# Optimization experiments

Hardware: AMD Instinct MI355X
Metric: run time of the kernel (lower is better)

## Reference

```python
import jax, jax.numpy as jnp
import numpy as np

B, NF, N, D, S, H = 16, 16, 1024, 128, 8, 128
EPS = 1e-8
SCALE = D ** -0.5


def _ln(x, g, b):
    m = x.mean(-1, keepdims=True)
    v = ((x - m) ** 2).mean(-1, keepdims=True)
    return (x - m) / jnp.sqrt(v + 1e-5) * g + b


def setup_inputs() -> dict:
    key = jax.random.key(0)
    ks = jax.random.split(key, 16)
    w = lambda k, *s: jax.random.normal(k, s, jnp.float32) * 0.02
    return {
        'inputs': jax.random.normal(ks[0], (B, NF, N, D), jnp.float32),
        'slots_init': jax.random.normal(ks[1], (1, S, D), jnp.float32),
        'Wq': w(ks[2], D, D), 'bq': jnp.zeros((D,), jnp.float32),
        'Wk': w(ks[3], D, D), 'bk': jnp.zeros((D,), jnp.float32),
        'Wv': w(ks[4], D, D), 'bv': jnp.zeros((D,), jnp.float32),
        'W1': w(ks[5], H, D), 'b1': jnp.zeros((H,), jnp.float32),
        'W2': w(ks[6], D, H), 'b2': jnp.zeros((D,), jnp.float32),
        'Wih': w(ks[7], 3 * D, D), 'Whh': w(ks[8], 3 * D, D),
        'bih': jnp.zeros((3 * D,), jnp.float32), 'bhh': jnp.zeros((3 * D,), jnp.float32),
        'g_in': jnp.ones((D,), jnp.float32), 'be_in': jnp.zeros((D,), jnp.float32),
        'g_sl': jnp.ones((D,), jnp.float32), 'be_sl': jnp.zeros((D,), jnp.float32),
        'g_ff': jnp.ones((D,), jnp.float32), 'be_ff': jnp.zeros((D,), jnp.float32),
    }


def reference(inputs, slots_init, Wq, bq, Wk, bk, Wv, bv, W1, b1, W2, b2,
              Wih, Whh, bih, bhh, g_in, be_in, g_sl, be_sl, g_ff, be_ff):
    def gru(x, h):  # PyTorch GRUCell, x/h: [BS, D]
        gi = x @ Wih.T + bih
        gh = h @ Whh.T + bhh
        r = jax.nn.sigmoid(gi[:, :D] + gh[:, :D])
        z = jax.nn.sigmoid(gi[:, D:2 * D] + gh[:, D:2 * D])
        n = jnp.tanh(gi[:, 2 * D:] + r * gh[:, 2 * D:])
        return (1.0 - z) * n + z * h

    def get_attention(slots, x):  # slots [B,S,D], x [B,N,D]
        slots_prev = slots
        xn = _ln(x, g_in, be_in)
        k = xn @ Wk.T + bk
        v = xn @ Wv.T + bv
        q = _ln(slots, g_sl, be_sl) @ Wq.T + bq
        dots = jnp.einsum('bid,bjd->bij', q, k) * SCALE  # [B,S,N]
        attn_ori = jax.nn.softmax(dots, axis=1) + EPS    # softmax over slots
        attn = attn_ori / attn_ori.sum(axis=-1, keepdims=True)
        updates = jnp.einsum('bjd,bij->bid', v, attn)    # [B,S,D]
        slots = gru(updates.reshape(-1, D), slots_prev.reshape(-1, D)).reshape(slots.shape[0], -1, D)
        ff = jax.nn.relu(_ln(slots, g_ff, be_ff) @ W1.T + b1) @ W2.T + b2
        return slots + ff, attn_ori

    slots = jnp.broadcast_to(slots_init, (inputs.shape[0], S, D))
    slots, _ = get_attention(slots, inputs[:, 0])  # warm-up on frame 0

    def body(carry, x_f):
        s, a = get_attention(carry, x_f)
        return s, (s, a)

    _, (slots_seq, attn_seq) = jax.lax.scan(body, slots, jnp.moveaxis(inputs, 1, 0))
    slots_out = jnp.moveaxis(slots_seq, 0, 1)  # [B,NF,S,D]
    attns = jnp.moveaxis(attn_seq, 0, 1)       # [B,NF,S,N]
    return slots_out, attns
```

## Files before the change

kernel.cpp:

```cpp
#include <hip/hip_runtime.h>

#define B_ 16
#define NF_ 16
#define N_ 1024
#define D_ 128
#define S_ 8
#define SCALE_ 0.08838834764831845f
#define NB 256
#define NT 512

struct SmemA {
  float Xt[64 * 132];
  float qWs[1024];
  float at[512];
  float rowsum[64], rowsum2[64];
  float qbs[8];
};
struct SmemB {
  float Pk[128];
  float gh[384];
  float gi[384];
  float hn[128], buf[128], hid[128], nrm[128];
  float red[8];
  float ssm;
};
union Smem { SmemA a; SmemB b; };

__device__ __forceinline__ float gload(const float* p) {
  return __hip_atomic_load(p, __ATOMIC_RELAXED, __HIP_MEMORY_SCOPE_AGENT);
}
__device__ __forceinline__ void gstore(float* p, float v) {
  __hip_atomic_store(p, v, __ATOMIC_RELAXED, __HIP_MEMORY_SCOPE_AGENT);
}

__device__ __forceinline__ void arrive(unsigned* c) {
  __syncthreads();
  if (threadIdx.x == 0) {
    __builtin_amdgcn_s_waitcnt(0);
    __hip_atomic_fetch_add(c, 1u, __ATOMIC_RELAXED, __HIP_MEMORY_SCOPE_AGENT);
  }
}
__device__ __forceinline__ void wait_for(unsigned* c, unsigned target) {
  if (threadIdx.x == 0) {
    while (__hip_atomic_load(c, __ATOMIC_RELAXED, __HIP_MEMORY_SCOPE_AGENT) < target)
      __builtin_amdgcn_s_sleep(1);
  }
  __syncthreads();
}

__device__ __forceinline__ float dot128f(const float* __restrict__ wrow, const float* x, float acc) {
  const float4* w = (const float4*)wrow;
#pragma unroll
  for (int i = 0; i < 32; ++i) {
    float4 v = w[i];
    const float4 xv = *(const float4*)(x + i * 4);
    acc += v.x * xv.x + v.y * xv.y + v.z * xv.z + v.w * xv.w;
  }
  return acc;
}

__device__ __forceinline__ void stats128(float v, int t, float* red, float& m, float& inv, float eps) {
  __syncthreads();
  float s = (t < 128) ? v : 0.f;
  float s2 = (t < 128) ? v * v : 0.f;
#pragma unroll
  for (int off = 32; off; off >>= 1) { s += __shfl_down(s, off); s2 += __shfl_down(s2, off); }
  if (t == 0)  { red[0] = s; red[2] = s2; }
  if (t == 64) { red[1] = s; red[3] = s2; }
  __syncthreads();
  m = (red[0] + red[1]) * (1.f / 128.f);
  float var = (red[2] + red[3]) * (1.f / 128.f) - m * m;
  inv = rsqrtf(var + 1e-5f);
}

__device__ __forceinline__ float sigm(float x) { return 1.f / (1.f + __expf(-x)); }
__device__ __forceinline__ float tanh_f(float x) { return 1.f - 2.f / (1.f + __expf(2.f * x)); }

__device__ void q_project(SmemB& Bm, const float* slot,
    const float* __restrict__ g_sl, const float* __restrict__ be_sl,
    const float* __restrict__ Wqk, const float* __restrict__ bqk,
    const float* __restrict__ wqbk, const float* __restrict__ bqbk,
    float* qW_g, float* qb_g, int bs) {
  int t = threadIdx.x;
  float m, inv;
  float sv = (t < 128) ? slot[t] : 0.f;
  stats128(sv, t, Bm.red, m, inv, 1e-5f);
  if (t < 128) Bm.nrm[t] = (sv - m) * inv * g_sl[t] + be_sl[t];
  __syncthreads();
  if (t < 128) {
    float a = dot128f(Wqk + t * 128, Bm.nrm, bqk[t]);
    gstore(&qW_g[bs * 128 + t], a);
    float p = wqbk[t] * Bm.nrm[t];
#pragma unroll
    for (int off = 32; off; off >>= 1) p += __shfl_down(p, off);
    if (t == 0)  Bm.red[4] = p;
    if (t == 64) Bm.red[5] = p;
  }
  __syncthreads();
  if (t == 0) gstore(&qb_g[bs], Bm.red[4] + Bm.red[5] + bqbk[0]);
}

__global__ __launch_bounds__(128) void precomp(
    const float* __restrict__ Wih, const float* __restrict__ bih,
    const float* __restrict__ Wv, const float* __restrict__ bv,
    const float* __restrict__ Wq, const float* __restrict__ bq,
    const float* __restrict__ Wk, const float* __restrict__ bk,
    float* Wiv, float* bihv, float* Wqk, float* bqk, float* wqbk, float* bqbk) {
  __shared__ float r2[2];
  int r = blockIdx.x, t = threadIdx.x;
  if (r < 384) {
    float acc = 0.f;
#pragma unroll 8
    for (int k = 0; k < 128; ++k) acc += Wih[r * 128 + k] * Wv[k * 128 + t];
    Wiv[r * 128 + t] = acc;
    float p = Wih[r * 128 + t] * bv[t];
#pragma unroll
    for (int off = 32; off; off >>= 1) p += __shfl_down(p, off);
    if ((t & 63) == 0) r2[t >> 6] = p;
    __syncthreads();
    if (t == 0) bihv[r] = r2[0] + r2[1] + bih[r];
  } else {
    int c = r - 384;
    float acc = 0.f;
#pragma unroll 8
    for (int dd = 0; dd < 128; ++dd) acc += Wk[dd * 128 + c] * Wq[dd * 128 + t];
    Wqk[c * 128 + t] = acc;
    float p = Wk[t * 128 + c] * bq[t];
#pragma unroll
    for (int off = 32; off; off >>= 1) p += __shfl_down(p, off);
    if ((t & 63) == 0) r2[t >> 6] = p;
    __syncthreads();
    if (t == 0) bqk[c] = r2[0] + r2[1];
    if (c == 0) {
      float a2 = 0.f;
#pragma unroll 8
      for (int dd = 0; dd < 128; ++dd) a2 += Wq[dd * 128 + t] * bk[dd];
      wqbk[t] = a2;
      float p2 = bq[t] * bk[t];
#pragma unroll
      for (int off = 32; off; off >>= 1) p2 += __shfl_down(p2, off);
      __syncthreads();
      if ((t & 63) == 0) r2[t >> 6] = p2;
      __syncthreads();
      if (t == 0) bqbk[0] = r2[0] + r2[1];
    }
  }
}

__global__ __launch_bounds__(NT) void slot_persist(
    const float* __restrict__ x, const float* __restrict__ slots_init,
    const float* __restrict__ Whh, const float* __restrict__ bhh,
    const float* __restrict__ W1, const float* __restrict__ b1,
    const float* __restrict__ W2, const float* __restrict__ b2,
    const float* __restrict__ g_in, const float* __restrict__ be_in,
    const float* __restrict__ g_sl, const float* __restrict__ be_sl,
    const float* __restrict__ g_ff, const float* __restrict__ be_ff,
    const float* __restrict__ Wiv, const float* __restrict__ bihv,
    const float* __restrict__ Wqk, const float* __restrict__ bqk,
    const float* __restrict__ wqbk, const float* __restrict__ bqbk,
    float* out_slots, float* out_attn,
    unsigned* cntA, unsigned* cntB,
    float* qW_g, float* qb_g, float* P_part, float* S_part) {
  __shared__ __align__(16) Smem sm;
  __shared__ __align__(16) float slot_sh[128];
  __shared__ __align__(16) float gs[128], bs_[128];
  int t = threadIdx.x, bid = blockIdx.x;
  int b = bid >> 4, jt = bid & 15;
  bool isB = (jt < 8);
  unsigned* cA = cntA + (b << 6);
  unsigned* cB = cntB + (b << 6);

  if (t < 128) { gs[t] = g_in[t]; bs_[t] = be_in[t]; }
  if (isB) {
    if (t < 128) slot_sh[t] = slots_init[jt * 128 + t];
    q_project(sm.b, slot_sh, g_sl, be_sl, Wqk, bqk, wqbk, bqbk, qW_g, qb_g, b * 8 + jt);
    arrive(cB);
  }
  float4 pf[4];
  {
    const float* xsrc = x + (((long)b * NF_ + 0) * N_ + jt * 64) * D_;
#pragma unroll
    for (int i = 0; i < 4; ++i) {
      int ch = t + i * 512;
      pf[i] = *(const float4*)(xsrc + (ch >> 5) * 128 + (ch & 31) * 4);
    }
  }
  wait_for(cB, 8u);

  for (int it = 0; it < 17; ++it) {
    int f = (it == 0) ? 0 : it - 1;
    int wo = it > 0;
#pragma unroll
    for (int i = 0; i < 4; ++i) {
      int ch = t + i * 512;
      *(float4*)&sm.a.Xt[(ch >> 5) * 132 + (ch & 31) * 4] = pf[i];
    }
    sm.a.qWs[t] = gload(&qW_g[b * 1024 + t]);
    sm.a.qWs[512 + t] = gload(&qW_g[b * 1024 + 512 + t]);
    if (t < 8) sm.a.qbs[t] = gload(&qb_g[b * 8 + t]);
    __syncthreads();
    int r8 = t >> 3, p8 = t & 7;
    {
      const float4* row4 = (const float4*)(sm.a.Xt + r8 * 132 + p8 * 16);
      float s1 = 0.f, s2 = 0.f;
#pragma unroll
      for (int i = 0; i < 4; ++i) {
        float4 v = row4[i];
        s1 += v.x + v.y + v.z + v.w;
        s2 += v.x * v.x + v.y * v.y + v.z * v.z + v.w * v.w;
      }
      s1 += __shfl_down(s1, 1); s2 += __shfl_down(s2, 1);
      s1 += __shfl_down(s1, 2); s2 += __shfl_down(s2, 2);
      s1 += __shfl_down(s1, 4); s2 += __shfl_down(s2, 4);
      if (p8 == 0) { sm.a.rowsum[r8] = s1; sm.a.rowsum2[r8] = s2; }
    }
    __syncthreads();
    {
      float m = sm.a.rowsum[r8] * (1.f / 128.f);
      float var = sm.a.rowsum2[r8] * (1.f / 128.f) - m * m;
      float inv = rsqrtf(var + 1e-5f);
      float4* row4 = (float4*)(sm.a.Xt + r8 * 132 + p8 * 16);
      const float4* gg4 = (const float4*)(gs + p8 * 16);
      const float4* bb4 = (const float4*)(bs_ + p8 * 16);
#pragma unroll
      for (int i = 0; i < 4; ++i) {
        float4 v = row4[i], g4 = gg4[i], b4 = bb4[i];
        v.x = (v.x - m) * inv * g4.x + b4.x;
        v.y = (v.y - m) * inv * g4.y + b4.y;
        v.z = (v.z - m) * inv * g4.z + b4.z;
        v.w = (v.w - m) * inv * g4.w + b4.w;
        row4[i] = v;
      }
    }
    __syncthreads();
    {
      int s = t >> 6, j = t & 63;
      const float4* qq4 = (const float4*)(sm.a.qWs + s * 128);
      const float4* xr4 = (const float4*)(sm.a.Xt + j * 132);
      float d = 0.f;
#pragma unroll
      for (int k = 0; k < 32; ++k) {
        float4 xv = xr4[k], qv = qq4[k];
        d += xv.x * qv.x + xv.y * qv.y + xv.z * qv.z + xv.w * qv.w;
      }
      sm.a.at[s * 64 + j] = (d + sm.a.qbs[s]) * SCALE_;
    }
    __syncthreads();
    if (t < 64) {
      float vals[8], mx = -1e30f;
#pragma unroll
      for (int s = 0; s < 8; ++s) { vals[s] = sm.a.at[s * 64 + t]; mx = fmaxf(mx, vals[s]); }
      float sum = 0.f;
#pragma unroll
      for (int s = 0; s < 8; ++s) { vals[s] = __expf(vals[s] - mx); sum += vals[s]; }
      float rr = 1.f / sum;
#pragma unroll
      for (int s = 0; s < 8; ++s) { vals[s] = vals[s] * rr + 1e-8f; sm.a.at[s * 64 + t] = vals[s]; }
      if (wo) {
#pragma unroll
        for (int s = 0; s < 8; ++s)
          out_attn[(((long)b * NF_ + f) * S_ + s) * N_ + jt * 64 + t] = vals[s];
      }
    }
    __syncthreads();
    {
      int w = t >> 6, lane = t & 63;
      float v = sm.a.at[w * 64 + lane];
#pragma unroll
      for (int off = 32; off; off >>= 1) v += __shfl_down(v, off);
      if (lane == 0) gstore(&S_part[(b * 16 + jt) * 8 + w], v);
    }
    {
      int k2 = t & 127, h = t >> 7;
      float u0 = 0.f, u1 = 0.f;
      const float* a0 = sm.a.at + h * 64;
      const float* a1 = sm.a.at + (h + 4) * 64;
#pragma unroll
      for (int j0 = 0; j0 < 64; j0 += 4) {
        float4 av0 = *(const float4*)(a0 + j0);
        float4 av1 = *(const float4*)(a1 + j0);
        float x0 = sm.a.Xt[(j0 + 0) * 132 + k2];
        float x1 = sm.a.Xt[(j0 + 1) * 132 + k2];
        float x2 = sm.a.Xt[(j0 + 2) * 132 + k2];
        float x3 = sm.a.Xt[(j0 + 3) * 132 + k2];
        u0 += av0.x * x0 + av0.y * x1 + av0.z * x2 + av0.w * x3;
        u1 += av1.x * x0 + av1.y * x1 + av1.z * x2 + av1.w * x3;
      }
      float* pp = P_part + (long)(b * 16 + jt) * 8 * 128;
      gstore(&pp[h * 128 + k2], u0);
      gstore(&pp[(h + 4) * 128 + k2], u1);
    }
    arrive(cA);
    if (it < 16) {
      const float* xsrc = x + (((long)b * NF_ + it) * N_ + jt * 64) * D_;
#pragma unroll
      for (int i = 0; i < 4; ++i) {
        int ch = t + i * 512;
        pf[i] = *(const float4*)(xsrc + (ch >> 5) * 128 + (ch & 31) * 4);
      }
    }
    if (isB) {
      wait_for(cA, 16u * (it + 1));
      SmemB& Bm = sm.b;
      int s = jt;
      if (t < 128) {
        float pa = 0.f;
#pragma unroll
        for (int j = 0; j < 16; ++j)
          pa += gload(&P_part[(long)((b * 16 + j) * 8 + s) * 128 + t]);
        Bm.Pk[t] = pa;
      } else {
        int r = t - 128;
        Bm.gh[r] = dot128f(Whh + r * 128, slot_sh, bhh[r]);
      }
      __syncthreads();
      if (t < 384) {
        Bm.gi[t] = dot128f(Wiv + (long)t * 128, Bm.Pk, 0.f);
      } else if (t >= 448 && t < 464) {
        int tl = t - 448;
        float sv = gload(&S_part[(b * 16 + tl) * 8 + s]);
        sv += __shfl_down(sv, 8); sv += __shfl_down(sv, 4);
        sv += __shfl_down(sv, 2); sv += __shfl_down(sv, 1);
        if (tl == 0) Bm.ssm = sv;
      }
      __syncthreads();
      if (t < 128) {
        float invss = 1.f / Bm.ssm;
        float gr = sigm(Bm.gi[t] * invss + bihv[t] + Bm.gh[t]);
        float gz = sigm(Bm.gi[128 + t] * invss + bihv[128 + t] + Bm.gh[128 + t]);
        float gn = tanh_f(Bm.gi[256 + t] * invss + bihv[256 + t] + gr * Bm.gh[256 + t]);
        Bm.hn[t] = (1.f - gz) * gn + gz * slot_sh[t];
      }
      float m, inv;
      float hv = (t < 128) ? Bm.hn[t] : 0.f;
      stats128(hv, t, Bm.red, m, inv, 1e-5f);
      if (t < 128) Bm.buf[t] = (hv - m) * inv * g_ff[t] + be_ff[t];
      __syncthreads();
      if (t < 128) Bm.hid[t] = fmaxf(dot128f(W1 + t * 128, Bm.buf, b1[t]), 0.f);
      __syncthreads();
      if (t < 128) {
        float ffv = dot128f(W2 + t * 128, Bm.hid, b2[t]);
        float sn = Bm.hn[t] + ffv;
        slot_sh[t] = sn;
        if (wo) out_slots[(((long)b * NF_ + f) * S_ + s) * D_ + t] = sn;
      }
      __syncthreads();
      if (it < 16) {
        q_project(Bm, slot_sh, g_sl, be_sl, Wqk, bqk, wqbk, bqbk, qW_g, qb_g, b * 8 + s);
        arrive(cB);
        wait_for(cB, 8u * (it + 2));
      }
    } else {
      if (it < 16) wait_for(cB, 8u * (it + 2));
    }
  }
}

extern "C" void kernel_launch(void* const* d_in, const int* in_sizes, int n_in,
                              void* d_out, int out_size, void* d_ws, size_t ws_size,
                              hipStream_t stream) {
  const float* inputs     = (const float*)d_in[0];
  const float* slots_init = (const float*)d_in[1];
  const float* Wq  = (const float*)d_in[2];
  const float* bq  = (const float*)d_in[3];
  const float* Wk  = (const float*)d_in[4];
  const float* bk  = (const float*)d_in[5];
  const float* Wv  = (const float*)d_in[6];
  const float* bv  = (const float*)d_in[7];
  const float* W1  = (const float*)d_in[8];
  const float* b1  = (const float*)d_in[9];
  const float* W2  = (const float*)d_in[10];
  const float* b2  = (const float*)d_in[11];
  const float* Wih = (const float*)d_in[12];
  const float* Whh = (const float*)d_in[13];
  const float* bih = (const float*)d_in[14];
  const float* bhh = (const float*)d_in[15];
  const float* g_in  = (const float*)d_in[16];
  const float* be_in = (const float*)d_in[17];
  const float* g_sl  = (const float*)d_in[18];
  const float* be_sl = (const float*)d_in[19];
  const float* g_ff  = (const float*)d_in[20];
  const float* be_ff = (const float*)d_in[21];

  float* out_slots = (float*)d_out;
  float* out_attn  = out_slots + (size_t)B_ * NF_ * S_ * D_;

  char* ws = (char*)d_ws;
  unsigned* cntA = (unsigned*)ws;
  unsigned* cntB = (unsigned*)(ws + 4096);
  float* Wiv   = (float*)(ws + 16384);
  float* bihv  = (float*)(ws + 212992);
  float* WqkW  = (float*)(ws + 214528);
  float* bqk   = (float*)(ws + 280064);
  float* wqbk  = (float*)(ws + 280576);
  float* bqbk  = (float*)(ws + 281088);
  float* qW_g  = (float*)(ws + 281344);
  float* qb_g  = (float*)(ws + 346880);
  float* P_part = (float*)(ws + 347392);
  float* S_part = (float*)(ws + 1395968);

  hipMemsetAsync(d_ws, 0, 16384, stream);

  precomp<<<512, 128, 0, stream>>>(Wih, bih, Wv, bv, Wq, bq, Wk, bk,
                                   Wiv, bihv, WqkW, bqk, wqbk, bqbk);
  slot_persist<<<NB, NT, 0, stream>>>(inputs, slots_init, Whh, bhh,
      W1, b1, W2, b2, g_in, be_in, g_sl, be_sl, g_ff, be_ff,
      Wiv, bihv, WqkW, bqk, wqbk, bqbk,
      out_slots, out_attn, cntA, cntB, qW_g, qb_g, P_part, S_part);
}
```

Before: 716.9 us.

## Fold input LayerNorm into query and update reductions, use atomic accumulation

Instead of normalizing each 64x128 input tile in shared memory, the kernel folds the LayerNorm gain into the published query vector. It applies per-row mean and rstd algebraically in the dot product and in the weighted update sum. Row statistics are computed straight from the prefetched registers, and the tile is stored with an XOR swizzle instead of padding. Per-block partial updates are accumulated with atomics into double-buffered global arrays, so the slot blocks no longer sum 16 partials. The wait for new queries moves to the top of the next iteration so the next frame's prefetch overlaps the GRU/MLP phase. The trade-off is more atomic traffic and a larger workspace memset.

```diff
diff --git a/kernel.cpp b/kernel.cpp
--- a/kernel.cpp
+++ b/kernel.cpp
@@ -10,21 +10,19 @@
 #define NT 512
 
 struct SmemA {
-  float Xt[64 * 132];
-  float qWs[1024];
-  float at[512];
-  float rowsum[64], rowsum2[64];
-  float qbs[8];
+  float Xt[64 * 128];
+  float at[8 * 64];
+  float gqWs[1024];
+  float mean[64], rinv[64];
+  float c1s[8], c0s[8];
 };
 struct SmemB {
   float Pk[128];
   float gh[384];
   float gi[384];
   float hn[128], buf[128], hid[128], nrm[128];
-  float red[8];
-  float ssm;
+  float red[16];
 };
-union Smem { SmemA a; SmemB b; };
 
 __device__ __forceinline__ float gload(const float* p) {
   return __hip_atomic_load(p, __ATOMIC_RELAXED, __HIP_MEMORY_SCOPE_AGENT);
@@ -32,7 +30,6 @@
 __device__ __forceinline__ void gstore(float* p, float v) {
   __hip_atomic_store(p, v, __ATOMIC_RELAXED, __HIP_MEMORY_SCOPE_AGENT);
 }
-
 __device__ __forceinline__ void arrive(unsigned* c) {
   __syncthreads();
   if (threadIdx.x == 0) {
@@ -76,28 +73,64 @@
 __device__ __forceinline__ float sigm(float x) { return 1.f / (1.f + __expf(-x)); }
 __device__ __forceinline__ float tanh_f(float x) { return 1.f - 2.f / (1.f + __expf(2.f * x)); }
 
-__device__ void q_project(SmemB& Bm, const float* slot,
+__device__ __forceinline__ void stage_stats(const float4* pf, float* Xt, float* mean, float* rinv, int t) {
+  float s1[4], s2[4];
+#pragma unroll
+  for (int i = 0; i < 4; ++i) {
+    int r = (t >> 5) + i * 16, kg = t & 31;
+    *(float4*)&Xt[r * 128 + ((kg ^ (r & 7)) << 2)] = pf[i];
+    s1[i] = pf[i].x + pf[i].y + pf[i].z + pf[i].w;
+    s2[i] = pf[i].x * pf[i].x + pf[i].y * pf[i].y + pf[i].z * pf[i].z + pf[i].w * pf[i].w;
+  }
+#pragma unroll
+  for (int mk = 16; mk; mk >>= 1) {
+#pragma unroll
+    for (int i = 0; i < 4; ++i) { s1[i] += __shfl_xor(s1[i], mk); s2[i] += __shfl_xor(s2[i], mk); }
+  }
+  if ((t & 31) == 0) {
+#pragma unroll
+    for (int i = 0; i < 4; ++i) {
+      int r = (t >> 5) + i * 16;
+      float mm = s1[i] * (1.f / 128.f);
+      mean[r] = mm;
+      rinv[r] = rsqrtf(s2[i] * (1.f / 128.f) - mm * mm + 1e-5f);
+    }
+  }
+}
+
+__device__ void q_project_pub(SmemB& Bm, const float* slot,
     const float* __restrict__ g_sl, const float* __restrict__ be_sl,
     const float* __restrict__ Wqk, const float* __restrict__ bqk,
     const float* __restrict__ wqbk, const float* __restrict__ bqbk,
-    float* qW_g, float* qb_g, int bs) {
-  int t = threadIdx.x;
+    const float* gI, const float* bI,
+    float* gqW_g, float* cc_g, int b, int s, int t) {
   float m, inv;
   float sv = (t < 128) ? slot[t] : 0.f;
   stats128(sv, t, Bm.red, m, inv, 1e-5f);
   if (t < 128) Bm.nrm[t] = (sv - m) * inv * g_sl[t] + be_sl[t];
   __syncthreads();
   if (t < 128) {
-    float a = dot128f(Wqk + t * 128, Bm.nrm, bqk[t]);
-    gstore(&qW_g[bs * 128 + t], a);
-    float p = wqbk[t] * Bm.nrm[t];
-#pragma unroll
-    for (int off = 32; off; off >>= 1) p += __shfl_down(p, off);
-    if (t == 0)  Bm.red[4] = p;
-    if (t == 64) Bm.red[5] = p;
-  }
-  __syncthreads();
-  if (t == 0) gstore(&qb_g[bs], Bm.red[4] + Bm.red[5] + bqbk[0]);
+    float qv = dot128f(Wqk + t * 128, Bm.nrm, bqk[t]);
+    float gq = gI[t] * qv;
+    gstore(&gqW_g[b * 1024 + s * 128 + t], gq);
+    float r0 = gq, r1 = bI[t] * qv, r2 = wqbk[t] * Bm.nrm[t];
+#pragma unroll
+    for (int off = 32; off; off >>= 1) {
+      r0 += __shfl_down(r0, off); r1 += __shfl_down(r1, off); r2 += __shfl_down(r2, off);
+    }
+    if ((t & 63) == 0) {
+      int w = t >> 6;
+      Bm.red[8 + w] = r0; Bm.red[10 + w] = r1; Bm.red[12 + w] = r2;
+    }
+  }
+  __syncthreads();
+  if (t == 0) {
+    float c1 = Bm.red[8] + Bm.red[9];
+    float qb = Bm.red[12] + Bm.red[13] + bqbk[0];
+    float c0 = Bm.red[10] + Bm.red[11] + qb;
+    gstore(&cc_g[b * 16 + s], c1);
+    gstore(&cc_g[b * 16 + 8 + s], c0);
+  }
 }
 
 __global__ __launch_bounds__(128) void precomp(
@@ -160,8 +193,9 @@
     const float* __restrict__ wqbk, const float* __restrict__ bqbk,
     float* out_slots, float* out_attn,
     unsigned* cntA, unsigned* cntB,
-    float* qW_g, float* qb_g, float* P_part, float* S_part) {
-  __shared__ __align__(16) Smem sm;
+    float* U_g, float* SMB_g, float* gqW_g, float* cc_g) {
+  __shared__ __align__(16) SmemA sa;
+  __shared__ __align__(16) SmemB sb;
   __shared__ __align__(16) float slot_sh[128];
   __shared__ __align__(16) float gs[128], bs_[128];
   int t = threadIdx.x, bid = blockIdx.x;
@@ -169,11 +203,14 @@
   bool isB = (jt < 8);
   unsigned* cA = cntA + (b << 6);
   unsigned* cB = cntB + (b << 6);
+  int s = t >> 6, j = t & 63;
 
   if (t < 128) { gs[t] = g_in[t]; bs_[t] = be_in[t]; }
+  __syncthreads();
   if (isB) {
     if (t < 128) slot_sh[t] = slots_init[jt * 128 + t];
-    q_project(sm.b, slot_sh, g_sl, be_sl, Wqk, bqk, wqbk, bqbk, qW_g, qb_g, b * 8 + jt);
+    q_project_pub(sb, slot_sh, g_sl, be_sl, Wqk, bqk, wqbk, bqbk, gs, bs_,
+                  gqW_g, cc_g, b, jt, t);
     arrive(cB);
   }
   float4 pf[4];
@@ -185,112 +222,136 @@
       pf[i] = *(const float4*)(xsrc + (ch >> 5) * 128 + (ch & 31) * 4);
     }
   }
-  wait_for(cB, 8u);
+  stage_stats(pf, sa.Xt, sa.mean, sa.rinv, t);
 
   for (int it = 0; it < 17; ++it) {
     int f = (it == 0) ? 0 : it - 1;
     int wo = it > 0;
-#pragma unroll
-    for (int i = 0; i < 4; ++i) {
-      int ch = t + i * 512;
-      *(float4*)&sm.a.Xt[(ch >> 5) * 132 + (ch & 31) * 4] = pf[i];
-    }
-    sm.a.qWs[t] = gload(&qW_g[b * 1024 + t]);
-    sm.a.qWs[512 + t] = gload(&qW_g[b * 1024 + 512 + t]);
-    if (t < 8) sm.a.qbs[t] = gload(&qb_g[b * 8 + t]);
-    __syncthreads();
-    int r8 = t >> 3, p8 = t & 7;
-    {
-      const float4* row4 = (const float4*)(sm.a.Xt + r8 * 132 + p8 * 16);
-      float s1 = 0.f, s2 = 0.f;
-#pragma unroll
-      for (int i = 0; i < 4; ++i) {
-        float4 v = row4[i];
-        s1 += v.x + v.y + v.z + v.w;
-        s2 += v.x * v.x + v.y * v.y + v.z * v.z + v.w * v.w;
-      }
-      s1 += __shfl_down(s1, 1); s2 += __shfl_down(s2, 1);
-      s1 += __shfl_down(s1, 2); s2 += __shfl_down(s2, 2);
-      s1 += __shfl_down(s1, 4); s2 += __shfl_down(s2, 4);
-      if (p8 == 0) { sm.a.rowsum[r8] = s1; sm.a.rowsum2[r8] = s2; }
-    }
+    int par = it & 1;
+    wait_for(cB, 8u * (it + 1));
+    sa.gqWs[t] = gload(&gqW_g[b * 1024 + t]);
+    sa.gqWs[512 + t] = gload(&gqW_g[b * 1024 + 512 + t]);
+    if (t < 8) sa.c1s[t] = gload(&cc_g[b * 16 + t]);
+    else if (t < 16) sa.c0s[t - 8] = gload(&cc_g[b * 16 + t]);
     __syncthreads();
     {
-      float m = sm.a.rowsum[r8] * (1.f / 128.f);
-      float var = sm.a.rowsum2[r8] * (1.f / 128.f) - m * m;
-      float inv = rsqrtf(var + 1e-5f);
-      float4* row4 = (float4*)(sm.a.Xt + r8 * 132 + p8 * 16);
-      const float4* gg4 = (const float4*)(gs + p8 * 16);
-      const float4* bb4 = (const float4*)(bs_ + p8 * 16);
-#pragma unroll
-      for (int i = 0; i < 4; ++i) {
-        float4 v = row4[i], g4 = gg4[i], b4 = bb4[i];
-        v.x = (v.x - m) * inv * g4.x + b4.x;
-        v.y = (v.y - m) * inv * g4.y + b4.y;
-        v.z = (v.z - m) * inv * g4.z + b4.z;
-        v.w = (v.w - m) * inv * g4.w + b4.w;
-        row4[i] = v;
-      }
-    }
-    __syncthreads();
-    {
-      int s = t >> 6, j = t & 63;
-      const float4* qq4 = (const float4*)(sm.a.qWs + s * 128);
-      const float4* xr4 = (const float4*)(sm.a.Xt + j * 132);
+      const float4* qq4 = (const float4*)(sa.gqWs + s * 128);
       float d = 0.f;
 #pragma unroll
-      for (int k = 0; k < 32; ++k) {
-        float4 xv = xr4[k], qv = qq4[k];
+      for (int k4 = 0; k4 < 32; ++k4) {
+        float4 xv = *(const float4*)&sa.Xt[j * 128 + ((k4 ^ (j & 7)) << 2)];
+        float4 qv = qq4[k4];
         d += xv.x * qv.x + xv.y * qv.y + xv.z * qv.z + xv.w * qv.w;
       }
-      sm.a.at[s * 64 + j] = (d + sm.a.qbs[s]) * SCALE_;
+      float val = (d - sa.mean[j] * sa.c1s[s]) * sa.rinv[j] + sa.c0s[s];
+      sa.at[s * 64 + j] = val * SCALE_;
     }
     __syncthreads();
     if (t < 64) {
       float vals[8], mx = -1e30f;
 #pragma unroll
-      for (int s = 0; s < 8; ++s) { vals[s] = sm.a.at[s * 64 + t]; mx = fmaxf(mx, vals[s]); }
+      for (int ss = 0; ss < 8; ++ss) { vals[ss] = sa.at[ss * 64 + t]; mx = fmaxf(mx, vals[ss]); }
       float sum = 0.f;
 #pragma unroll
-      for (int s = 0; s < 8; ++s) { vals[s] = __expf(vals[s] - mx); sum += vals[s]; }
+      for (int ss = 0; ss < 8; ++ss) { vals[ss] = __expf(vals[ss] - mx); sum += vals[ss]; }
       float rr = 1.f / sum;
 #pragma unroll
-      for (int s = 0; s < 8; ++s) { vals[s] = vals[s] * rr + 1e-8f; sm.a.at[s * 64 + t] = vals[s]; }
+      for (int ss = 0; ss < 8; ++ss) { vals[ss] = vals[ss] * rr + 1e-8f; sa.at[ss * 64 + t] = vals[ss]; }
       if (wo) {
 #pragma unroll
-        for (int s = 0; s < 8; ++s)
-          out_attn[(((long)b * NF_ + f) * S_ + s) * N_ + jt * 64 + t] = vals[s];
+        for (int ss = 0; ss < 8; ++ss)
+          out_attn[(((long)b * NF_ + f) * S_ + ss) * N_ + jt * 64 + t] = vals[ss];
       }
     }
     __syncthreads();
     {
-      int w = t >> 6, lane = t & 63;
-      float v = sm.a.at[w * 64 + lane];
-#pragma unroll
-      for (int off = 32; off; off >>= 1) v += __shfl_down(v, off);
-      if (lane == 0) gstore(&S_part[(b * 16 + jt) * 8 + w], v);
+      float v = sa.at[s * 64 + j];
+      float vm = v * sa.mean[j] * sa.rinv[j];
+#pragma unroll
+      for (int off = 32; off; off >>= 1) { v += __shfl_down(v, off); vm += __shfl_down(vm, off); }
+      if (j == 0) {
+        float* smb = SMB_g + (b * 2 + par) * 16;
+        atomicAdd(&smb[s], v);
+        atomicAdd(&smb[8 + s], vm);
+      }
     }
     {
       int k2 = t & 127, h = t >> 7;
+      int dg = k2 >> 2, dr = k2 & 3;
       float u0 = 0.f, u1 = 0.f;
-      const float* a0 = sm.a.at + h * 64;
-      const float* a1 = sm.a.at + (h + 4) * 64;
+      const float* a0 = sa.at + h * 64;
+      const float* a1 = sa.at + (h + 4) * 64;
 #pragma unroll
       for (int j0 = 0; j0 < 64; j0 += 4) {
         float4 av0 = *(const float4*)(a0 + j0);
         float4 av1 = *(const float4*)(a1 + j0);
-        float x0 = sm.a.Xt[(j0 + 0) * 132 + k2];
-        float x1 = sm.a.Xt[(j0 + 1) * 132 + k2];
-        float x2 = sm.a.Xt[(j0 + 2) * 132 + k2];
-        float x3 = sm.a.Xt[(j0 + 3) * 132 + k2];
-        u0 += av0.x * x0 + av0.y * x1 + av0.z * x2 + av0.w * x3;
-        u1 += av1.x * x0 + av1.y * x1 + av1.z * x2 + av1.w * x3;
-      }
-      float* pp = P_part + (long)(b * 16 + jt) * 8 * 128;
-      gstore(&pp[h * 128 + k2], u0);
-      gstore(&pp[(h + 4) * 128 + k2], u1);
+        float4 rv = *(const float4*)(sa.rinv + j0);
+        float x0 = sa.Xt[(j0 + 0) * 128 + ((dg ^ ((j0 + 0) & 7)) << 2) + dr];
+        float x1 = sa.Xt[(j0 + 1) * 128 + ((dg ^ ((j0 + 1) & 7)) << 2) + dr];
+        float x2 = sa.Xt[(j0 + 2) * 128 + ((dg ^ ((j0 + 2) & 7)) << 2) + dr];
+        float x3 = sa.Xt[(j0 + 3) * 128 + ((dg ^ ((j0 + 3) & 7)) << 2) + dr];
+        float rx0 = rv.x * x0, rx1 = rv.y * x1, rx2 = rv.z * x2, rx3 = rv.w * x3;
+        u0 += av0.x * rx0 + av0.y * rx1 + av0.z * rx2 + av0.w * rx3;
+        u1 += av1.x * rx0 + av1.y * rx1 + av1.z * rx2 + av1.w * rx3;
+      }
+      float* Ub = U_g + ((b * 2 + par) << 10);
+      atomicAdd(&Ub[h * 128 + k2], u0);
+      atomicAdd(&Ub[(h + 4) * 128 + k2], u1);
     }
     arrive(cA);
+    if (isB) {
+      wait_for(cA, 16u * (it + 1));
+      int sl = jt;
+      float* Ub = U_g + ((b * 2 + par) << 10);
+      float* smb = SMB_g + (b * 2 + par) * 16;
+      if (t < 128) {
+        sb.Pk[t] = gload(&Ub[sl * 128 + t]);
+        if (t == 0) {
+          sb.red[14] = gload(&smb[sl]);
+          sb.red[15] = gload(&smb[8 + sl]);
+        }
+      } else {
+        int r = t - 128;
+        sb.gh[r] = dot128f(Whh + r * 128, slot_sh, bhh[r]);
+      }
+      __syncthreads();
+      float ssv = sb.red[14], mbv = sb.red[15];
+      if (t < 128) {
+        sb.Pk[t] = gs[t] * (sb.Pk[t] - mbv) + bs_[t] * ssv;
+        gstore(&Ub[sl * 128 + t], 0.f);
+        if (t == 0) { gstore(&smb[sl], 0.f); gstore(&smb[8 + sl], 0.f); }
+      }
+      __syncthreads();
+      if (t < 384) sb.gi[t] = dot128f(Wiv + (long)t * 128, sb.Pk, 0.f);
+      __syncthreads();
+      float hnew = 0.f;
+      if (t < 128) {
+        float invss = 1.f / ssv;
+        float gr = sigm(sb.gi[t] * invss + bihv[t] + sb.gh[t]);
+        float gz = sigm(sb.gi[128 + t] * invss + bihv[128 + t] + sb.gh[128 + t]);
+        float gn = tanh_f(sb.gi[256 + t] * invss + bihv[256 + t] + gr * sb.gh[256 + t]);
+        hnew = (1.f - gz) * gn + gz * slot_sh[t];
+        sb.hn[t] = hnew;
+      }
+      float m, inv;
+      stats128(hnew, t, sb.red, m, inv, 1e-5f);
+      if (t < 128) sb.buf[t] = (hnew - m) * inv * g_ff[t] + be_ff[t];
+      __syncthreads();
+      if (t < 128) sb.hid[t] = fmaxf(dot128f(W1 + t * 128, sb.buf, b1[t]), 0.f);
+      __syncthreads();
+      if (t < 128) {
+        float ffv = dot128f(W2 + t * 128, sb.hid, b2[t]);
+        float sn = sb.hn[t] + ffv;
+        slot_sh[t] = sn;
+        if (wo) out_slots[(((long)b * NF_ + f) * S_ + sl) * D_ + t] = sn;
+      }
+      __syncthreads();
+      if (it < 16) {
+        q_project_pub(sb, slot_sh, g_sl, be_sl, Wqk, bqk, wqbk, bqbk, gs, bs_,
+                      gqW_g, cc_g, b, sl, t);
+        arrive(cB);
+      }
+    }
     if (it < 16) {
       const float* xsrc = x + (((long)b * NF_ + it) * N_ + jt * 64) * D_;
 #pragma unroll
@@ -298,60 +359,7 @@
         int ch = t + i * 512;
         pf[i] = *(const float4*)(xsrc + (ch >> 5) * 128 + (ch & 31) * 4);
       }
-    }
-    if (isB) {
-      wait_for(cA, 16u * (it + 1));
-      SmemB& Bm = sm.b;
-      int s = jt;
-      if (t < 128) {
-        float pa = 0.f;
-#pragma unroll
-        for (int j = 0; j < 16; ++j)
-          pa += gload(&P_part[(long)((b * 16 + j) * 8 + s) * 128 + t]);
-        Bm.Pk[t] = pa;
-      } else {
-        int r = t - 128;
-        Bm.gh[r] = dot128f(Whh + r * 128, slot_sh, bhh[r]);
-      }
-      __syncthreads();
-      if (t < 384) {
-        Bm.gi[t] = dot128f(Wiv + (long)t * 128, Bm.Pk, 0.f);
-      } else if (t >= 448 && t < 464) {
-        int tl = t - 448;
-        float sv = gload(&S_part[(b * 16 + tl) * 8 + s]);
-        sv += __shfl_down(sv, 8); sv += __shfl_down(sv, 4);
-        sv += __shfl_down(sv, 2); sv += __shfl_down(sv, 1);
-        if (tl == 0) Bm.ssm = sv;
-      }
-      __syncthreads();
-      if (t < 128) {
-        float invss = 1.f / Bm.ssm;
-        float gr = sigm(Bm.gi[t] * invss + bihv[t] + Bm.gh[t]);
-        float gz = sigm(Bm.gi[128 + t] * invss + bihv[128 + t] + Bm.gh[128 + t]);
-        float gn = tanh_f(Bm.gi[256 + t] * invss + bihv[256 + t] + gr * Bm.gh[256 + t]);
-        Bm.hn[t] = (1.f - gz) * gn + gz * slot_sh[t];
-      }
-      float m, inv;
-      float hv = (t < 128) ? Bm.hn[t] : 0.f;
-      stats128(hv, t, Bm.red, m, inv, 1e-5f);
-      if (t < 128) Bm.buf[t] = (hv - m) * inv * g_ff[t] + be_ff[t];
-      __syncthreads();
-      if (t < 128) Bm.hid[t] = fmaxf(dot128f(W1 + t * 128, Bm.buf, b1[t]), 0.f);
-      __syncthreads();
-      if (t < 128) {
-        float ffv = dot128f(W2 + t * 128, Bm.hid, b2[t]);
-        float sn = Bm.hn[t] + ffv;
-        slot_sh[t] = sn;
-        if (wo) out_slots[(((long)b * NF_ + f) * S_ + s) * D_ + t] = sn;
-      }
-      __syncthreads();
-      if (it < 16) {
-        q_project(Bm, slot_sh, g_sl, be_sl, Wqk, bqk, wqbk, bqbk, qW_g, qb_g, b * 8 + s);
-        arrive(cB);
-        wait_for(cB, 8u * (it + 2));
-      }
-    } else {
-      if (it < 16) wait_for(cB, 8u * (it + 2));
+      stage_stats(pf, sa.Xt, sa.mean, sa.rinv, t);
     }
   }
 }
@@ -388,23 +396,23 @@
   char* ws = (char*)d_ws;
   unsigned* cntA = (unsigned*)ws;
   unsigned* cntB = (unsigned*)(ws + 4096);
-  float* Wiv   = (float*)(ws + 16384);
-  float* bihv  = (float*)(ws + 212992);
-  float* WqkW  = (float*)(ws + 214528);
-  float* bqk   = (float*)(ws + 280064);
-  float* wqbk  = (float*)(ws + 280576);
-  float* bqbk  = (float*)(ws + 281088);
-  float* qW_g  = (float*)(ws + 281344);
-  float* qb_g  = (float*)(ws + 346880);
-  float* P_part = (float*)(ws + 347392);
-  float* S_part = (float*)(ws + 1395968);
-
-  hipMemsetAsync(d_ws, 0, 16384, stream);
+  float* U_g   = (float*)(ws + 8192);
+  float* SMB_g = (float*)(ws + 139264);
+  float* Wiv   = (float*)(ws + 141312);
+  float* bihv  = (float*)(ws + 337920);
+  float* WqkW  = (float*)(ws + 339456);
+  float* bqk   = (float*)(ws + 404992);
+  float* wqbk  = (float*)(ws + 405504);
+  float* bqbk  = (float*)(ws + 406016);
+  float* gqW_g = (float*)(ws + 406272);
+  float* cc_g  = (float*)(ws + 471808);
+
+  hipMemsetAsync(d_ws, 0, 141312, stream);
 
   precomp<<<512, 128, 0, stream>>>(Wih, bih, Wv, bv, Wq, bq, Wk, bk,
                                    Wiv, bihv, WqkW, bqk, wqbk, bqbk);
   slot_persist<<<NB, NT, 0, stream>>>(inputs, slots_init, Whh, bhh,
       W1, b1, W2, b2, g_in, be_in, g_sl, be_sl, g_ff, be_ff,
       Wiv, bihv, WqkW, bqk, wqbk, bqbk,
-      out_slots, out_attn, cntA, cntB, qW_g, qb_g, P_part, S_part);
-}
+      out_slots, out_attn, cntA, cntB, U_g, SMB_g, gqW_g, cc_g);
+}
```

Result: no change. 712.2 us (-0.6%).
